# Performance work log

Hardware: AMD Instinct MI355X
Metric: run time of the kernel (lower is better)

Reference implementation:

```python
import jax, jax.numpy as jnp
import numpy as np

SR = 16000
NFFT = 512
HOP = 256
NMELS = 64
NFREQ = NFFT // 2 + 1  # 257
BATCH = 32
WAVE_LEN = 960000  # 60 s at 16 kHz


def _mel_matrix():
    # librosa.filters.mel(sr=16000, n_fft=512, n_mels=64, fmin=20, fmax=8000, htk=True, norm=None).T
    def hz2mel(f):
        return 2595.0 * np.log10(1.0 + np.asarray(f, dtype=np.float64) / 700.0)

    def mel2hz(m):
        return 700.0 * (10.0 ** (np.asarray(m, dtype=np.float64) / 2595.0) - 1.0)

    mel_pts = np.linspace(hz2mel(20.0), hz2mel(8000.0), NMELS + 2)
    hz_pts = mel2hz(mel_pts)                      # [n_mels+2]
    fft_freqs = np.linspace(0.0, SR / 2.0, NFREQ)  # [257]
    fdiff = np.diff(hz_pts)
    ramps = hz_pts[:, None] - fft_freqs[None, :]
    lower = -ramps[:-2] / fdiff[:-1, None]
    upper = ramps[2:] / fdiff[1:, None]
    w = np.maximum(0.0, np.minimum(lower, upper))  # [n_mels, 257], norm=None
    return jnp.asarray(w.T.astype(np.float32))     # [257, n_mels]


def _stft_mag(x):
    # torch-stft style: reflect-pad by n_fft//2, hann window (periodic), hop=256
    pad = NFFT // 2
    xp = jnp.pad(x, ((0, 0), (pad, pad)), mode='reflect')  # [B, L+2*pad]
    n_frames = (xp.shape[1] - NFFT) // HOP + 1
    idx = np.arange(n_frames)[:, None] * HOP + np.arange(NFFT)[None, :]  # [T, NFFT]
    frames = xp[:, idx]  # [B, T, NFFT]
    win = (0.5 - 0.5 * np.cos(2.0 * np.pi * np.arange(NFFT) / NFFT)).astype(np.float32)
    spec = jnp.fft.rfft(frames * win, axis=-1)  # [B, T, 257] complex
    re, im = jnp.real(spec), jnp.imag(spec)
    return jnp.sqrt(re * re + im * im)  # (spec**2).sum(-1).sqrt()


def setup_inputs() -> dict:
    key = jax.random.key(0)
    wav = jax.random.normal(key, (BATCH, WAVE_LEN), dtype=jnp.float32)
    alpha = jnp.full((1, NFREQ), 3.0, dtype=jnp.float32)  # nn.init.constant_(self.alpha, 3)
    return {"input_waveform": wav, "alpha": alpha, "mel_matrix": _mel_matrix()}


def reference(input_waveform, alpha, mel_matrix):
    mag = _stft_mag(input_waveform)          # [B, T, F]
    a = jax.nn.sigmoid(alpha)[0]             # [F]

    # EMA recurrence: tmp = a*tmp + (1-a)*mag[:, i], tmp0 = mag[:, 0]
    def step(carry, x_t):
        c = a * carry + (1.0 - a) * x_t
        return c, c

    mag_t = jnp.moveaxis(mag, 1, 0)          # [T, B, F] time-major for scan
    _, avg_t = jax.lax.scan(step, mag[:, 0, :], mag_t)
    avg_mag = jnp.moveaxis(avg_t, 0, 1)      # [B, T, F]

    norm_mag = mag / (avg_mag + 1e-8)
    abs_mel = jnp.matmul(norm_mag, mel_matrix) + 1e-6  # [B, T, n_mels]
    return abs_mel
```

## Files before the change

### kernel.cpp

```cpp
#include <hip/hip_runtime.h>
#include <math.h>

#define NFFT      512
#define HOP       256
#define NBINS     257
#define NMELS     64
#define BATCH     32
#define WAVE_LEN  960000
#define NFRAMES   3751
#define NPAIRS    1876
#define CHUNK     128
#define NCHUNK    30
#define MROWS     (BATCH * NFRAMES)
#define KPAD      288

#define PI2F 6.283185307179586f

typedef unsigned short ushort_t;
typedef __attribute__((ext_vector_type(8))) short bf16x8;
typedef __attribute__((ext_vector_type(4))) float f32x4;

__device__ __forceinline__ float sigmoidf_(float x) { return 1.0f / (1.0f + __expf(-x)); }

__device__ __forceinline__ ushort_t f2b(float x) {
  unsigned u = __float_as_uint(x);
  u = u + 0x7FFFu + ((u >> 16) & 1u);
  return (ushort_t)(u >> 16);
}
__device__ __forceinline__ float b2f(ushort_t h) {
  return __uint_as_float(((unsigned)h) << 16);
}

__global__ __launch_bounds__(512) void init_tables(const float* __restrict__ mel,
                                                   float* __restrict__ win,
                                                   float* __restrict__ twA,
                                                   float* __restrict__ twB,
                                                   ushort_t* __restrict__ melbT) {
  const int n = threadIdx.x;
  win[n] = 0.5f - 0.5f * __cosf(PI2F * (float)n / (float)NFFT);
  {
    int j = n >> 6, p = n & 63;
    float ang = -PI2F * (float)(p * j) / 512.0f;
    twA[2 * n]     = __cosf(ang);
    twA[2 * n + 1] = __sinf(ang);
  }
  if (n < 64) {
    int p = n >> 3, j = n & 7;
    float ang = -PI2F * (float)(p * j) / 64.0f;
    twB[2 * n]     = __cosf(ang);
    twB[2 * n + 1] = __sinf(ang);
  }
  for (int i = n; i < NMELS * KPAD; i += 512) {
    int m = i / KPAD, k = i - m * KPAD;
    melbT[i] = (k < NBINS) ? f2b(mel[(size_t)k * NMELS + m]) : (ushort_t)0;
  }
}

__device__ __forceinline__ void fft8(float zr[8], float zi[8]) {
  float er[4], ei[4], orr[4], oi[4];
  {
    float Ar = zr[0] + zr[4], Ai = zi[0] + zi[4];
    float Br = zr[2] + zr[6], Bi = zi[2] + zi[6];
    float Cr = zr[0] - zr[4], Ci = zi[0] - zi[4];
    float dr = zr[2] - zr[6], di = zi[2] - zi[6];
    er[0] = Ar + Br; ei[0] = Ai + Bi;
    er[1] = Cr + di; ei[1] = Ci - dr;
    er[2] = Ar - Br; ei[2] = Ai - Bi;
    er[3] = Cr - di; ei[3] = Ci + dr;
  }
  {
    float Ar = zr[1] + zr[5], Ai = zi[1] + zi[5];
    float Br = zr[3] + zr[7], Bi = zi[3] + zi[7];
    float Cr = zr[1] - zr[5], Ci = zi[1] - zi[5];
    float dr = zr[3] - zr[7], di = zi[3] - zi[7];
    orr[0] = Ar + Br; oi[0] = Ai + Bi;
    orr[1] = Cr + di; oi[1] = Ci - dr;
    orr[2] = Ar - Br; oi[2] = Ai - Bi;
    orr[3] = Cr - di; oi[3] = Ci + dr;
  }
  const float R = 0.70710678118654752f;
  zr[0] = er[0] + orr[0]; zi[0] = ei[0] + oi[0];
  zr[4] = er[0] - orr[0]; zi[4] = ei[0] - oi[0];
  {
    float tr = R * (orr[1] + oi[1]);
    float ti = R * (oi[1] - orr[1]);
    zr[1] = er[1] + tr; zi[1] = ei[1] + ti;
    zr[5] = er[1] - tr; zi[5] = ei[1] - ti;
  }
  {
    float tr = oi[2], ti = -orr[2];
    zr[2] = er[2] + tr; zi[2] = ei[2] + ti;
    zr[6] = er[2] - tr; zi[6] = ei[2] - ti;
  }
  {
    float tr = R * (oi[3] - orr[3]);
    float ti = -R * (orr[3] + oi[3]);
    zr[3] = er[3] + tr; zi[3] = ei[3] + ti;
    zr[7] = er[3] - tr; zi[7] = ei[3] - ti;
  }
}

__global__ __launch_bounds__(64) void stft_kernel(const float* __restrict__ wav,
                                                  const float* __restrict__ win,
                                                  const float* __restrict__ twA,
                                                  const float* __restrict__ twB,
                                                  ushort_t* __restrict__ mag) {
  const int pr  = blockIdx.x;
  const int b   = blockIdx.y;
  const int tid = threadIdx.x;

  __shared__ float sre[576], sim[576];

  const float* w = wav + (size_t)b * WAVE_LEN;
  const int f0 = 2 * pr, f1 = f0 + 1;
  const bool has1 = (f1 < NFRAMES);
  const int base0 = f0 * HOP - (NFFT / 2);
  const int base1 = base0 + HOP;

  float zr[8], zi[8];
#pragma unroll
  for (int j = 0; j < 8; ++j) {
    int n = tid + 64 * j;
    float wn = win[n];
    int p0 = base0 + n;
    p0 = (p0 < 0) ? -p0 : p0;
    p0 = (p0 >= WAVE_LEN) ? (2 * WAVE_LEN - 2 - p0) : p0;
    float x0 = w[p0];
    float x1 = has1 ? w[base1 + n] : 0.0f;
    zr[j] = x0 * wn;
    zi[j] = x1 * wn;
  }

  fft8(zr, zi);
  const float2* twA2 = (const float2*)twA;
#pragma unroll
  for (int j = 1; j < 8; ++j) {
    float2 t = twA2[j * 64 + tid];
    float r = zr[j] * t.x - zi[j] * t.y;
    zi[j]   = zi[j] * t.x + zr[j] * t.y;
    zr[j]   = r;
  }

#pragma unroll
  for (int j = 0; j < 8; ++j) {
    int n = tid + 64 * j;
    int a = n + (n >> 3);
    sre[a] = zr[j]; sim[a] = zi[j];
  }
  __syncthreads();
  const int g = tid >> 3, q = tid & 7;
#pragma unroll
  for (int j = 0; j < 8; ++j) {
    int n = g * 64 + q + 8 * j;
    int a = n + (n >> 3);
    zr[j] = sre[a]; zi[j] = sim[a];
  }

  fft8(zr, zi);
  const float2* twB2 = (const float2*)twB;
#pragma unroll
  for (int j = 1; j < 8; ++j) {
    float2 t = twB2[q * 8 + j];
    float r = zr[j] * t.x - zi[j] * t.y;
    zi[j]   = zi[j] * t.x + zr[j] * t.y;
    zr[j]   = r;
  }

  __syncthreads();
#pragma unroll
  for (int j = 0; j < 8; ++j) {
    int n = g * 64 + q + 8 * j;
    int a = n + (n >> 3);
    sre[a] = zr[j]; sim[a] = zi[j];
  }
  __syncthreads();
#pragma unroll
  for (int j = 0; j < 8; ++j) {
    int n = 8 * tid + j;
    int a = n + (n >> 3);
    zr[j] = sre[a]; zi[j] = sim[a];
  }

  fft8(zr, zi);

  __syncthreads();
#pragma unroll
  for (int j = 0; j < 8; ++j) {
    int k = 64 * j + 8 * q + g;
    sre[k] = zr[j]; sim[k] = zi[j];
  }
  __syncthreads();

  ushort_t* out0 = mag + ((size_t)b * NFRAMES + f0) * NBINS;
  ushort_t* out1 = out0 + NBINS;
  for (int k = tid; k <= 256; k += 64) {
    int kn = (NFFT - k) & (NFFT - 1);
    float ar = sre[k],  ai = sim[k];
    float br = sre[kn], bi = sim[kn];
    float xr = ar + br, xi = ai - bi;
    float yr = ai + bi, yi = ar - br;
    out0[k] = f2b(0.5f * sqrtf(xr * xr + xi * xi));
    if (has1) out1[k] = f2b(0.5f * sqrtf(yr * yr + yi * yi));
  }
}

__global__ void scan_partial(const ushort_t* __restrict__ mag,
                             const float* __restrict__ alpha,
                             float* __restrict__ Bc) {
  const int c = blockIdx.x, b = blockIdx.y, f = threadIdx.x;
  if (f >= NBINS) return;
  const float a = sigmoidf_(alpha[f]);
  const float om = 1.0f - a;
  const int t0 = c * CHUNK;
  const int t1 = min(NFRAMES, t0 + CHUNK);
  const ushort_t* p = mag + ((size_t)b * NFRAMES + t0) * NBINS + f;
  float v = 0.0f;
  for (int t = t0; t < t1; ++t) {
    v = fmaf(a, v, om * b2f(*p));
    p += NBINS;
  }
  Bc[((size_t)b * NBINS + f) * NCHUNK + c] = v;
}

__global__ void scan_combine(const ushort_t* __restrict__ mag,
                             const float* __restrict__ alpha,
                             const float* __restrict__ Bc,
                             float* __restrict__ carry) {
  const int b = blockIdx.x, f = threadIdx.x;
  if (f >= NBINS) return;
  const float a = sigmoidf_(alpha[f]);
  float aL = a;
#pragma unroll
  for (int i = 0; i < 7; ++i) aL *= aL;
  float v = b2f(mag[(size_t)b * NFRAMES * NBINS + f]);
  const size_t off = ((size_t)b * NBINS + f) * NCHUNK;
  for (int c = 0; c < NCHUNK; ++c) {
    carry[off + c] = v;
    v = fmaf(aL, v, Bc[off + c]);
  }
}

__global__ void scan_apply(const ushort_t* __restrict__ mag,
                           const float* __restrict__ alpha,
                           const float* __restrict__ carry,
                           ushort_t* __restrict__ normb) {
  const int c = blockIdx.x, b = blockIdx.y, f = threadIdx.x;
  if (f >= KPAD) return;
  const int t0 = c * CHUNK;
  const int t1 = min(NFRAMES, t0 + CHUNK);
  if (f >= NBINS) {
    ushort_t* q = normb + ((size_t)b * NFRAMES + t0) * KPAD + f;
    for (int t = t0; t < t1; ++t) { *q = 0; q += KPAD; }
    return;
  }
  const float a = sigmoidf_(alpha[f]);
  const float om = 1.0f - a;
  float v = carry[((size_t)b * NBINS + f) * NCHUNK + c];
  const ushort_t* p = mag + ((size_t)b * NFRAMES + t0) * NBINS + f;
  ushort_t* q = normb + ((size_t)b * NFRAMES + t0) * KPAD + f;
  for (int t = t0; t < t1; ++t) {
    float m = b2f(*p);
    v = fmaf(a, v, om * m);
    *q = f2b(m / (v + 1e-8f));
    p += NBINS;
    q += KPAD;
  }
}

__global__ __launch_bounds__(256) void mel_gemm_mfma(const ushort_t* __restrict__ normb,
                                                     const ushort_t* __restrict__ melbT,
                                                     float* __restrict__ out) {
  const int wave = threadIdx.x >> 6;
  const int lane = threadIdx.x & 63;
  const int rt = blockIdx.x * 4 + wave;
  if (rt * 16 >= MROWS) return;
  const int row0 = rt * 16;
  const int m    = lane & 15;
  const int quad = lane >> 4;

  const ushort_t* Ap = normb + (size_t)(row0 + m) * KPAD + quad * 8;

  f32x4 acc[4];
#pragma unroll
  for (int ct = 0; ct < 4; ++ct) acc[ct] = (f32x4){0.f, 0.f, 0.f, 0.f};

#pragma unroll
  for (int ks = 0; ks < 9; ++ks) {
    bf16x8 a = *(const bf16x8*)(Ap + ks * 32);
#pragma unroll
    for (int ct = 0; ct < 4; ++ct) {
      bf16x8 bb = *(const bf16x8*)(melbT + (size_t)(ct * 16 + m) * KPAD + ks * 32 + quad * 8);
      acc[ct] = __builtin_amdgcn_mfma_f32_16x16x32_bf16(a, bb, acc[ct], 0, 0, 0);
    }
  }

#pragma unroll
  for (int ct = 0; ct < 4; ++ct) {
#pragma unroll
    for (int r = 0; r < 4; ++r) {
      int row = row0 + quad * 4 + r;
      out[(size_t)row * NMELS + ct * 16 + m] = acc[ct][r] + 1e-6f;
    }
  }
}

extern "C" void kernel_launch(void* const* d_in, const int* in_sizes, int n_in,
                              void* d_out, int out_size, void* d_ws, size_t ws_size,
                              hipStream_t stream) {
  const float* wav   = (const float*)d_in[0];
  const float* alpha = (const float*)d_in[1];
  const float* mel   = (const float*)d_in[2];
  float* out = (float*)d_out;

  ushort_t* magb  = (ushort_t*)d_ws;
  ushort_t* normb = magb + (size_t)BATCH * NFRAMES * NBINS;
  ushort_t* melbT = normb + (size_t)MROWS * KPAD;
  float* Bc    = (float*)(melbT + (size_t)NMELS * KPAD);
  float* carry = Bc + (size_t)BATCH * NBINS * NCHUNK;
  float* win   = carry + (size_t)BATCH * NBINS * NCHUNK;
  float* twA   = win + 512;
  float* twB   = twA + 1024;

  init_tables<<<1, 512, 0, stream>>>(mel, win, twA, twB, melbT);
  stft_kernel<<<dim3(NPAIRS, BATCH), 64, 0, stream>>>(wav, win, twA, twB, magb);
  scan_partial<<<dim3(NCHUNK, BATCH), 320, 0, stream>>>(magb, alpha, Bc);
  scan_combine<<<BATCH, 320, 0, stream>>>(magb, alpha, Bc, carry);
  scan_apply<<<dim3(NCHUNK, BATCH), 320, 0, stream>>>(magb, alpha, carry, normb);
  mel_gemm_mfma<<<(MROWS + 63) / 64, 256, 0, stream>>>(normb, melbT, out);
}
```

Before: 340.2 us.

## Fuse EMA scan-apply with mel GEMM through LDS and halve scan chunk

The scan-apply kernel and the mel MFMA GEMM are merged into one kernel. Each block computes the normalized bf16 magnitudes for a 64-frame chunk into shared memory and multiplies them by the mel matrix directly, so the padded normb intermediate is never written to or read back from global memory. The chunk size drops from 128 to 59 chunks of 64 (with the combine power adjusted to match), which raises block count and shortens the serial recurrence per thread. The STFT FFT code is also rewritten with float2 vectors and an interleaved complex LDS layout. Only 257 of 256 threads' worth of columns are active in the serial scan phase, and the LDS tile lowers occupancy.

```diff
diff --git a/kernel.cpp b/kernel.cpp
--- a/kernel.cpp
+++ b/kernel.cpp
@@ -9,14 +9,16 @@
 #define WAVE_LEN  960000
 #define NFRAMES   3751
 #define NPAIRS    1876
-#define CHUNK     128
-#define NCHUNK    30
+#define CHUNK     64
+#define NCHUNK    59
 #define MROWS     (BATCH * NFRAMES)
 #define KPAD      288
+#define LDSW      296
 
 #define PI2F 6.283185307179586f
 
 typedef unsigned short ushort_t;
+typedef __attribute__((ext_vector_type(2))) float f32x2;
 typedef __attribute__((ext_vector_type(8))) short bf16x8;
 typedef __attribute__((ext_vector_type(4))) float f32x4;
 
@@ -56,48 +58,32 @@
   }
 }
 
-__device__ __forceinline__ void fft8(float zr[8], float zi[8]) {
-  float er[4], ei[4], orr[4], oi[4];
+__device__ __forceinline__ f32x2 cmulw(f32x2 a, float c, float s) {
+  return (f32x2){a.x * c - a.y * s, a.y * c + a.x * s};
+}
+
+__device__ __forceinline__ void fft8v(f32x2 z[8]) {
+  f32x2 e[4], o[4];
   {
-    float Ar = zr[0] + zr[4], Ai = zi[0] + zi[4];
-    float Br = zr[2] + zr[6], Bi = zi[2] + zi[6];
-    float Cr = zr[0] - zr[4], Ci = zi[0] - zi[4];
-    float dr = zr[2] - zr[6], di = zi[2] - zi[6];
-    er[0] = Ar + Br; ei[0] = Ai + Bi;
-    er[1] = Cr + di; ei[1] = Ci - dr;
-    er[2] = Ar - Br; ei[2] = Ai - Bi;
-    er[3] = Cr - di; ei[3] = Ci + dr;
+    f32x2 A = z[0] + z[4], C = z[0] - z[4];
+    f32x2 B = z[2] + z[6], D = z[2] - z[6];
+    f32x2 Dn = (f32x2){D.y, -D.x};
+    e[0] = A + B; e[2] = A - B; e[1] = C + Dn; e[3] = C - Dn;
   }
   {
-    float Ar = zr[1] + zr[5], Ai = zi[1] + zi[5];
-    float Br = zr[3] + zr[7], Bi = zi[3] + zi[7];
-    float Cr = zr[1] - zr[5], Ci = zi[1] - zi[5];
-    float dr = zr[3] - zr[7], di = zi[3] - zi[7];
-    orr[0] = Ar + Br; oi[0] = Ai + Bi;
-    orr[1] = Cr + di; oi[1] = Ci - dr;
-    orr[2] = Ar - Br; oi[2] = Ai - Bi;
-    orr[3] = Cr - di; oi[3] = Ci + dr;
+    f32x2 A = z[1] + z[5], C = z[1] - z[5];
+    f32x2 B = z[3] + z[7], D = z[3] - z[7];
+    f32x2 Dn = (f32x2){D.y, -D.x};
+    o[0] = A + B; o[2] = A - B; o[1] = C + Dn; o[3] = C - Dn;
   }
   const float R = 0.70710678118654752f;
-  zr[0] = er[0] + orr[0]; zi[0] = ei[0] + oi[0];
-  zr[4] = er[0] - orr[0]; zi[4] = ei[0] - oi[0];
-  {
-    float tr = R * (orr[1] + oi[1]);
-    float ti = R * (oi[1] - orr[1]);
-    zr[1] = er[1] + tr; zi[1] = ei[1] + ti;
-    zr[5] = er[1] - tr; zi[5] = ei[1] - ti;
-  }
-  {
-    float tr = oi[2], ti = -orr[2];
-    zr[2] = er[2] + tr; zi[2] = ei[2] + ti;
-    zr[6] = er[2] - tr; zi[6] = ei[2] - ti;
-  }
-  {
-    float tr = R * (oi[3] - orr[3]);
-    float ti = -R * (orr[3] + oi[3]);
-    zr[3] = er[3] + tr; zi[3] = ei[3] + ti;
-    zr[7] = er[3] - tr; zi[7] = ei[3] - ti;
-  }
+  z[0] = e[0] + o[0]; z[4] = e[0] - o[0];
+  f32x2 t1 = (f32x2){R * (o[1].x + o[1].y), R * (o[1].y - o[1].x)};
+  z[1] = e[1] + t1; z[5] = e[1] - t1;
+  f32x2 t2 = (f32x2){o[2].y, -o[2].x};
+  z[2] = e[2] + t2; z[6] = e[2] - t2;
+  f32x2 t3 = (f32x2){R * (o[3].y - o[3].x), -R * (o[3].x + o[3].y)};
+  z[3] = e[3] + t3; z[7] = e[3] - t3;
 }
 
 __global__ __launch_bounds__(64) void stft_kernel(const float* __restrict__ wav,
@@ -109,7 +95,7 @@
   const int b   = blockIdx.y;
   const int tid = threadIdx.x;
 
-  __shared__ float sre[576], sim[576];
+  __shared__ f32x2 sz[576];
 
   const float* w = wav + (size_t)b * WAVE_LEN;
   const int f0 = 2 * pr, f1 = f0 + 1;
@@ -117,7 +103,7 @@
   const int base0 = f0 * HOP - (NFFT / 2);
   const int base1 = base0 + HOP;
 
-  float zr[8], zi[8];
+  f32x2 z[8];
 #pragma unroll
   for (int j = 0; j < 8; ++j) {
     int n = tid + 64 * j;
@@ -127,67 +113,57 @@
     p0 = (p0 >= WAVE_LEN) ? (2 * WAVE_LEN - 2 - p0) : p0;
     float x0 = w[p0];
     float x1 = has1 ? w[base1 + n] : 0.0f;
-    zr[j] = x0 * wn;
-    zi[j] = x1 * wn;
-  }
-
-  fft8(zr, zi);
+    z[j] = (f32x2){x0 * wn, x1 * wn};
+  }
+
+  fft8v(z);
   const float2* twA2 = (const float2*)twA;
 #pragma unroll
   for (int j = 1; j < 8; ++j) {
     float2 t = twA2[j * 64 + tid];
-    float r = zr[j] * t.x - zi[j] * t.y;
-    zi[j]   = zi[j] * t.x + zr[j] * t.y;
-    zr[j]   = r;
+    z[j] = cmulw(z[j], t.x, t.y);
   }
 
 #pragma unroll
   for (int j = 0; j < 8; ++j) {
     int n = tid + 64 * j;
-    int a = n + (n >> 3);
-    sre[a] = zr[j]; sim[a] = zi[j];
+    sz[n + (n >> 3)] = z[j];
   }
   __syncthreads();
   const int g = tid >> 3, q = tid & 7;
 #pragma unroll
   for (int j = 0; j < 8; ++j) {
     int n = g * 64 + q + 8 * j;
-    int a = n + (n >> 3);
-    zr[j] = sre[a]; zi[j] = sim[a];
-  }
-
-  fft8(zr, zi);
+    z[j] = sz[n + (n >> 3)];
+  }
+
+  fft8v(z);
   const float2* twB2 = (const float2*)twB;
 #pragma unroll
   for (int j = 1; j < 8; ++j) {
     float2 t = twB2[q * 8 + j];
-    float r = zr[j] * t.x - zi[j] * t.y;
-    zi[j]   = zi[j] * t.x + zr[j] * t.y;
-    zr[j]   = r;
+    z[j] = cmulw(z[j], t.x, t.y);
   }
 
   __syncthreads();
 #pragma unroll
   for (int j = 0; j < 8; ++j) {
     int n = g * 64 + q + 8 * j;
-    int a = n + (n >> 3);
-    sre[a] = zr[j]; sim[a] = zi[j];
-  }
-  __syncthreads();
-#pragma unroll
-  for (int j = 0; j < 8; ++j) {
-    int n = 8 * tid + j;
-    int a = n + (n >> 3);
-    zr[j] = sre[a]; zi[j] = sim[a];
-  }
-
-  fft8(zr, zi);
+    sz[n + (n >> 3)] = z[j];
+  }
+  __syncthreads();
+#pragma unroll
+  for (int j = 0; j < 8; ++j) {
+    z[j] = sz[9 * tid + j];
+  }
+
+  fft8v(z);
 
   __syncthreads();
 #pragma unroll
   for (int j = 0; j < 8; ++j) {
     int k = 64 * j + 8 * q + g;
-    sre[k] = zr[j]; sim[k] = zi[j];
+    sz[k] = z[j];
   }
   __syncthreads();
 
@@ -195,10 +171,9 @@
   ushort_t* out1 = out0 + NBINS;
   for (int k = tid; k <= 256; k += 64) {
     int kn = (NFFT - k) & (NFFT - 1);
-    float ar = sre[k],  ai = sim[k];
-    float br = sre[kn], bi = sim[kn];
-    float xr = ar + br, xi = ai - bi;
-    float yr = ai + bi, yi = ar - br;
+    f32x2 A = sz[k], B = sz[kn];
+    float xr = A.x + B.x, xi = A.y - B.y;
+    float yr = A.y + B.y, yi = A.x - B.x;
     out0[k] = f2b(0.5f * sqrtf(xr * xr + xi * xi));
     if (has1) out1[k] = f2b(0.5f * sqrtf(yr * yr + yi * yi));
   }
@@ -231,7 +206,7 @@
   const float a = sigmoidf_(alpha[f]);
   float aL = a;
 #pragma unroll
-  for (int i = 0; i < 7; ++i) aL *= aL;
+  for (int i = 0; i < 6; ++i) aL *= aL;
   float v = b2f(mag[(size_t)b * NFRAMES * NBINS + f]);
   const size_t off = ((size_t)b * NBINS + f) * NCHUNK;
   for (int c = 0; c < NCHUNK; ++c) {
@@ -240,45 +215,41 @@
   }
 }
 
-__global__ void scan_apply(const ushort_t* __restrict__ mag,
-                           const float* __restrict__ alpha,
-                           const float* __restrict__ carry,
-                           ushort_t* __restrict__ normb) {
-  const int c = blockIdx.x, b = blockIdx.y, f = threadIdx.x;
-  if (f >= KPAD) return;
+__global__ __launch_bounds__(256) void scan_gemm(const ushort_t* __restrict__ magb,
+                                                 const float* __restrict__ alpha,
+                                                 const float* __restrict__ carry,
+                                                 const ushort_t* __restrict__ melbT,
+                                                 float* __restrict__ out) {
+  const int c = blockIdx.x, b = blockIdx.y;
+  const int tid = threadIdx.x;
   const int t0 = c * CHUNK;
-  const int t1 = min(NFRAMES, t0 + CHUNK);
-  if (f >= NBINS) {
-    ushort_t* q = normb + ((size_t)b * NFRAMES + t0) * KPAD + f;
-    for (int t = t0; t < t1; ++t) { *q = 0; q += KPAD; }
-    return;
-  }
-  const float a = sigmoidf_(alpha[f]);
-  const float om = 1.0f - a;
-  float v = carry[((size_t)b * NBINS + f) * NCHUNK + c];
-  const ushort_t* p = mag + ((size_t)b * NFRAMES + t0) * NBINS + f;
-  ushort_t* q = normb + ((size_t)b * NFRAMES + t0) * KPAD + f;
-  for (int t = t0; t < t1; ++t) {
-    float m = b2f(*p);
-    v = fmaf(a, v, om * m);
-    *q = f2b(m / (v + 1e-8f));
-    p += NBINS;
-    q += KPAD;
-  }
-}
-
-__global__ __launch_bounds__(256) void mel_gemm_mfma(const ushort_t* __restrict__ normb,
-                                                     const ushort_t* __restrict__ melbT,
-                                                     float* __restrict__ out) {
-  const int wave = threadIdx.x >> 6;
-  const int lane = threadIdx.x & 63;
-  const int rt = blockIdx.x * 4 + wave;
-  if (rt * 16 >= MROWS) return;
-  const int row0 = rt * 16;
-  const int m    = lane & 15;
-  const int quad = lane >> 4;
-
-  const ushort_t* Ap = normb + (size_t)(row0 + m) * KPAD + quad * 8;
+  const int nv = min(CHUNK, NFRAMES - t0);
+
+  __shared__ __align__(16) ushort_t Ns[CHUNK][LDSW];
+
+  for (int f = tid; f < KPAD; f += 256) {
+    if (f < NBINS) {
+      const float a = sigmoidf_(alpha[f]);
+      const float om = 1.0f - a;
+      float v = carry[((size_t)b * NBINS + f) * NCHUNK + c];
+      const ushort_t* p = magb + ((size_t)b * NFRAMES + t0) * NBINS + f;
+      int t = 0;
+      for (; t < nv; ++t) {
+        float m = b2f(*p);
+        v = fmaf(a, v, om * m);
+        Ns[t][f] = f2b(m / (v + 1e-8f));
+        p += NBINS;
+      }
+      for (; t < CHUNK; ++t) Ns[t][f] = 0;
+    } else {
+      for (int t = 0; t < CHUNK; ++t) Ns[t][f] = 0;
+    }
+  }
+  __syncthreads();
+
+  const int wave = tid >> 6, lane = tid & 63;
+  const int m = lane & 15, quad = lane >> 4;
+  const int r0 = wave * 16;
 
   f32x4 acc[4];
 #pragma unroll
@@ -286,7 +257,7 @@
 
 #pragma unroll
   for (int ks = 0; ks < 9; ++ks) {
-    bf16x8 a = *(const bf16x8*)(Ap + ks * 32);
+    bf16x8 a = *(const bf16x8*)&Ns[r0 + m][ks * 32 + quad * 8];
 #pragma unroll
     for (int ct = 0; ct < 4; ++ct) {
       bf16x8 bb = *(const bf16x8*)(melbT + (size_t)(ct * 16 + m) * KPAD + ks * 32 + quad * 8);
@@ -298,8 +269,9 @@
   for (int ct = 0; ct < 4; ++ct) {
 #pragma unroll
     for (int r = 0; r < 4; ++r) {
-      int row = row0 + quad * 4 + r;
-      out[(size_t)row * NMELS + ct * 16 + m] = acc[ct][r] + 1e-6f;
+      int tl = r0 + quad * 4 + r;
+      if (t0 + tl < NFRAMES)
+        out[((size_t)b * NFRAMES + t0 + tl) * NMELS + ct * 16 + m] = acc[ct][r] + 1e-6f;
     }
   }
 }
@@ -313,8 +285,7 @@
   float* out = (float*)d_out;
 
   ushort_t* magb  = (ushort_t*)d_ws;
-  ushort_t* normb = magb + (size_t)BATCH * NFRAMES * NBINS;
-  ushort_t* melbT = normb + (size_t)MROWS * KPAD;
+  ushort_t* melbT = magb + (size_t)BATCH * NFRAMES * NBINS;
   float* Bc    = (float*)(melbT + (size_t)NMELS * KPAD);
   float* carry = Bc + (size_t)BATCH * NBINS * NCHUNK;
   float* win   = carry + (size_t)BATCH * NBINS * NCHUNK;
@@ -325,6 +296,5 @@
   stft_kernel<<<dim3(NPAIRS, BATCH), 64, 0, stream>>>(wav, win, twA, twB, magb);
   scan_partial<<<dim3(NCHUNK, BATCH), 320, 0, stream>>>(magb, alpha, Bc);
   scan_combine<<<BATCH, 320, 0, stream>>>(magb, alpha, Bc, carry);
-  scan_apply<<<dim3(NCHUNK, BATCH), 320, 0, stream>>>(magb, alpha, carry, normb);
-  mel_gemm_mfma<<<(MROWS + 63) / 64, 256, 0, stream>>>(normb, melbT, out);
-}
+  scan_gemm<<<dim3(NCHUNK, BATCH), 256, 0, stream>>>(magb, alpha, carry, melbT, out);
+}
```

New measurement: 315.5 us. 7.3% less time.
